# Kernel tuning notes

Measured on AMD Instinct MI355X. Metric: run time of the kernel, lower is better.

Reference implementation:

```python
import jax, jax.numpy as jnp
import numpy as np

B, S, D, H, DK, F, K = 8, 1024, 512, 8, 64, 2048, 31
EPS = 1e-5


def _ln(x, g, b):
    m = jnp.mean(x, -1, keepdims=True)
    v = jnp.mean((x - m) ** 2, -1, keepdims=True)
    return (x - m) * jax.lax.rsqrt(v + EPS) * g + b


def _ff(x, w1, b1, w2, b2):
    return jnp.maximum(x @ w1 + b1, 0.0) @ w2 + b2


def setup_inputs() -> dict:
    key = jax.random.key(0)
    ks = jax.random.split(key, 16)
    w = lambda k, shape: jax.random.normal(k, shape, dtype=jnp.float32) * 0.02
    inp = {"x": jax.random.normal(ks[0], (B, S, D), dtype=jnp.float32)}
    for name in ["norm1", "norm2", "norm3", "norm4", "conv_ln"]:
        inp[name + "_g"] = jnp.ones((D,), jnp.float32)
        inp[name + "_b"] = jnp.zeros((D,), jnp.float32)
    # feed-forward 1 and 2
    inp["ff1_w1"] = w(ks[1], (D, F)); inp["ff1_b1"] = jnp.zeros((F,), jnp.float32)
    inp["ff1_w2"] = w(ks[2], (F, D)); inp["ff1_b2"] = jnp.zeros((D,), jnp.float32)
    inp["ff2_w1"] = w(ks[3], (D, F)); inp["ff2_b1"] = jnp.zeros((F,), jnp.float32)
    inp["ff2_w2"] = w(ks[4], (F, D)); inp["ff2_b2"] = jnp.zeros((D,), jnp.float32)
    # attention projections ([in, out] layout)
    inp["wq"] = w(ks[5], (D, D)); inp["bq"] = jnp.zeros((D,), jnp.float32)
    inp["wk"] = w(ks[6], (D, D)); inp["bk"] = jnp.zeros((D,), jnp.float32)
    inp["wv"] = w(ks[7], (D, D)); inp["bv"] = jnp.zeros((D,), jnp.float32)
    inp["wo"] = w(ks[8], (D, D)); inp["bo"] = jnp.zeros((D,), jnp.float32)
    # convolution module
    inp["pw1_w"] = w(ks[9], (D, 2 * D)); inp["pw1_b"] = jnp.zeros((2 * D,), jnp.float32)
    inp["dw_w"] = w(ks[10], (D, 1, K)); inp["dw_b"] = jnp.zeros((D,), jnp.float32)
    inp["bn_g"] = jnp.ones((D,), jnp.float32); inp["bn_b"] = jnp.zeros((D,), jnp.float32)
    inp["bn_mean"] = jnp.zeros((D,), jnp.float32); inp["bn_var"] = jnp.ones((D,), jnp.float32)
    inp["pw2_w"] = w(ks[11], (D, D)); inp["pw2_b"] = jnp.zeros((D,), jnp.float32)
    return inp


def _forward(x, norm1_g, norm1_b, norm2_g, norm2_b, norm3_g, norm3_b, norm4_g, norm4_b,
             ff1_w1, ff1_b1, ff1_w2, ff1_b2, wq, bq, wk, bk, wv, bv, wo, bo,
             conv_ln_g, conv_ln_b, pw1_w, pw1_b, dw_w, dw_b,
             bn_g, bn_b, bn_mean, bn_var, pw2_w, pw2_b,
             ff2_w1, ff2_b1, ff2_w2, ff2_b2):
    b, s, _ = x.shape
    # half-step FF1
    x = x + 0.5 * _ff(_ln(x, norm1_g, norm1_b), ff1_w1, ff1_b1, ff1_w2, ff1_b2)
    # multi-head self-attention (pre-norm)
    h = _ln(x, norm2_g, norm2_b)
    q = (h @ wq + bq).reshape(b, s, H, DK)
    k = (h @ wk + bk).reshape(b, s, H, DK)
    v = (h @ wv + bv).reshape(b, s, H, DK)
    scores = jnp.einsum("bqhd,bkhd->bhqk", q, k) / jnp.sqrt(jnp.asarray(DK, x.dtype))
    attn = jax.nn.softmax(scores, axis=-1)
    o = jnp.einsum("bhqk,bkhd->bqhd", attn, v).reshape(b, s, D)
    x = x + (o @ wo + bo)
    # convolution module (pre-norm)
    h = _ln(x, norm3_g, norm3_b)
    h = _ln(h, conv_ln_g, conv_ln_b)
    h = h @ pw1_w + pw1_b                                 # [B,S,2D] pointwise conv1
    h = h[..., :D] * jax.nn.sigmoid(h[..., D:])           # GLU over channels
    h = h.transpose(0, 2, 1)                              # [B,D,S]
    h = jax.lax.conv_general_dilated(
        h, dw_w, window_strides=(1,), padding=((K // 2, K // 2),),
        feature_group_count=D, dimension_numbers=("NCH", "OIH", "NCH")) + dw_b[:, None]
    h = (h - bn_mean[:, None]) * jax.lax.rsqrt(bn_var + EPS)[:, None] * bn_g[:, None] + bn_b[:, None]
    h = h * jax.nn.sigmoid(h)                             # SiLU
    h = jnp.einsum("bcl,co->bol", h, pw2_w) + pw2_b[:, None]
    x = x + h.transpose(0, 2, 1)
    # half-step FF2
    x = x + 0.5 * _ff(_ln(x, norm4_g, norm4_b), ff2_w1, ff2_b1, ff2_w2, ff2_b2)
    return x


def reference(x, norm1_g, norm1_b, norm2_g, norm2_b, norm3_g, norm3_b, norm4_g, norm4_b,
              conv_ln_g, conv_ln_b, ff1_w1, ff1_b1, ff1_w2, ff1_b2,
              ff2_w1, ff2_b1, ff2_w2, ff2_b2, wq, bq, wk, bk, wv, bv, wo, bo,
              pw1_w, pw1_b, dw_w, dw_b, bn_g, bn_b, bn_mean, bn_var, pw2_w, pw2_b):
    return _forward(x, norm1_g, norm1_b, norm2_g, norm2_b, norm3_g, norm3_b, norm4_g, norm4_b,
                    ff1_w1, ff1_b1, ff1_w2, ff1_b2, wq, bq, wk, bk, wv, bv, wo, bo,
                    conv_ln_g, conv_ln_b, pw1_w, pw1_b, dw_w, dw_b,
                    bn_g, bn_b, bn_mean, bn_var, pw2_w, pw2_b,
                    ff2_w1, ff2_b1, ff2_w2, ff2_b2)
```

## Files before the change

kernel.cpp:

```cpp
#include <hip/hip_runtime.h>
#include <math.h>

#define TOK    8192
#define DMODEL 512
#define FDIM   2048
#define NH     8
#define DKH    64
#define SEQ    1024
#define BATCH  8
#define KCONV  31
#define LN_EPS 1e-5f

typedef __attribute__((ext_vector_type(8))) short bf16x8;
typedef __attribute__((ext_vector_type(4))) float f32x4;
typedef unsigned short ushort_t;

__device__ __forceinline__ float sigf(float x) { return 1.0f / (1.0f + __expf(-x)); }

__device__ __forceinline__ unsigned short f2bf(float f) {
  unsigned u = __float_as_uint(f);
  u = u + 0x7fffu + ((u >> 16) & 1u);
  return (unsigned short)(u >> 16);
}
__device__ __forceinline__ unsigned pk2(float a, float b) {
  return (unsigned)f2bf(a) | ((unsigned)f2bf(b) << 16);
}
__device__ __forceinline__ float bf2f(ushort_t u) {
  return __uint_as_float((unsigned)u << 16);
}

__device__ __forceinline__ void xcd_swizzle(int gx, int* bx, int* by) {
  const int nwg = gx * (int)gridDim.y;
  const int cpx = nwg >> 3;
  const int bid = (*by) * gx + (*bx);
  const int wg = (bid & 7) * cpx + (bid >> 3);
  *bx = wg % gx;
  *by = wg / gx;
}

struct WJob { const float* src; ushort_t* dst; int K, N, t0; };
struct WJobs { WJob j[10]; };

__global__ __launch_bounds__(256) void wcast_all(WJobs jobs) {
  __shared__ float tile[32][33];
  const int t = blockIdx.x;
  int i = 0;
#pragma unroll
  for (int k = 1; k < 10; ++k) if (t >= jobs.j[k].t0) i = k;
  const WJob jb = jobs.j[i];
  const int local = t - jb.t0;
  const int ntx = jb.N >> 5;
  const int bx = (local % ntx) * 32, by = (local / ntx) * 32;
  const int tx = threadIdx.x, ty = threadIdx.y;
#pragma unroll
  for (int r = 0; r < 32; r += 8)
    tile[ty + r][tx] = jb.src[(size_t)(by + ty + r) * jb.N + bx + tx];
  __syncthreads();
#pragma unroll
  for (int r = 0; r < 32; r += 8)
    jb.dst[(size_t)(bx + ty + r) * jb.K + by + tx] = f2bf(tile[tx][ty + r]);
}

__global__ void misc_prep(const float* __restrict__ w, float* __restrict__ wT,
                          const float* __restrict__ bq, const float* __restrict__ bk,
                          const float* __restrict__ bv, float* __restrict__ bcat) {
  const int idx = blockIdx.x * 256 + threadIdx.x;
  if (idx < DMODEL * KCONV) {
    const int d = idx / KCONV, k = idx % KCONV;
    wT[k * DMODEL + d] = w[idx];
  } else if (idx < DMODEL * KCONV + 3 * DMODEL) {
    const int c = idx - DMODEL * KCONV;
    bcat[c] = (c < DMODEL) ? bq[c] : (c < 2 * DMODEL ? bk[c - DMODEL] : bv[c - 2 * DMODEL]);
  }
}

template <bool OBF>
__global__ __launch_bounds__(256) void ln_kernel(const float* __restrict__ in,
                                                 const float* __restrict__ g,
                                                 const float* __restrict__ b,
                                                 void* __restrict__ outp) {
  const int wave = threadIdx.x >> 6, lane = threadIdx.x & 63;
  const size_t row = (size_t)blockIdx.x * 4 + wave;
  const float* p = in + row * DMODEL + lane * 8;
  const float4 v0 = *(const float4*)p;
  const float4 v1 = *(const float4*)(p + 4);
  float s  = v0.x + v0.y + v0.z + v0.w + v1.x + v1.y + v1.z + v1.w;
  float ss = v0.x*v0.x + v0.y*v0.y + v0.z*v0.z + v0.w*v0.w
           + v1.x*v1.x + v1.y*v1.y + v1.z*v1.z + v1.w*v1.w;
#pragma unroll
  for (int m = 1; m < 64; m <<= 1) { s += __shfl_xor(s, m); ss += __shfl_xor(ss, m); }
  const float mean = s * (1.0f / DMODEL);
  const float var  = ss * (1.0f / DMODEL) - mean * mean;
  const float rstd = rsqrtf(var + LN_EPS);
  const float4 g0 = *(const float4*)(g + lane * 8);
  const float4 g1 = *(const float4*)(g + lane * 8 + 4);
  const float4 bb0 = *(const float4*)(b + lane * 8);
  const float4 bb1 = *(const float4*)(b + lane * 8 + 4);
  float o[8];
  o[0] = (v0.x - mean) * rstd * g0.x + bb0.x;
  o[1] = (v0.y - mean) * rstd * g0.y + bb0.y;
  o[2] = (v0.z - mean) * rstd * g0.z + bb0.z;
  o[3] = (v0.w - mean) * rstd * g0.w + bb0.w;
  o[4] = (v1.x - mean) * rstd * g1.x + bb1.x;
  o[5] = (v1.y - mean) * rstd * g1.y + bb1.y;
  o[6] = (v1.z - mean) * rstd * g1.z + bb1.z;
  o[7] = (v1.w - mean) * rstd * g1.w + bb1.w;
  if (OBF) {
    uint4 pkv;
    pkv.x = pk2(o[0], o[1]); pkv.y = pk2(o[2], o[3]);
    pkv.z = pk2(o[4], o[5]); pkv.w = pk2(o[6], o[7]);
    *(uint4*)((ushort_t*)outp + row * DMODEL + lane * 8) = pkv;
  } else {
    float4 a, c;
    a.x = o[0]; a.y = o[1]; a.z = o[2]; a.w = o[3];
    c.x = o[4]; c.y = o[5]; c.z = o[6]; c.w = o[7];
    float* q = (float*)outp + row * DMODEL + lane * 8;
    *(float4*)q = a;
    *(float4*)(q + 4) = c;
  }
}

__global__ __launch_bounds__(256) void ln2_kernel(const float* __restrict__ in,
                                                  const float* __restrict__ g1,
                                                  const float* __restrict__ b1,
                                                  const float* __restrict__ g2,
                                                  const float* __restrict__ b2,
                                                  ushort_t* __restrict__ outp) {
  const int wave = threadIdx.x >> 6, lane = threadIdx.x & 63;
  const size_t row = (size_t)blockIdx.x * 4 + wave;
  const float* p = in + row * DMODEL + lane * 8;
  float v[8];
  {
    const float4 v0 = *(const float4*)p;
    const float4 v1 = *(const float4*)(p + 4);
    v[0]=v0.x; v[1]=v0.y; v[2]=v0.z; v[3]=v0.w;
    v[4]=v1.x; v[5]=v1.y; v[6]=v1.z; v[7]=v1.w;
  }
  float s = 0.f, ss = 0.f;
#pragma unroll
  for (int e = 0; e < 8; ++e) { s += v[e]; ss += v[e]*v[e]; }
#pragma unroll
  for (int m = 1; m < 64; m <<= 1) { s += __shfl_xor(s, m); ss += __shfl_xor(ss, m); }
  float mean = s * (1.0f / DMODEL);
  float rstd = rsqrtf(ss * (1.0f / DMODEL) - mean * mean + LN_EPS);
  const float4 ga = *(const float4*)(g1 + lane * 8);
  const float4 gb = *(const float4*)(g1 + lane * 8 + 4);
  const float4 ba = *(const float4*)(b1 + lane * 8);
  const float4 bb = *(const float4*)(b1 + lane * 8 + 4);
  const float gg1[8] = {ga.x,ga.y,ga.z,ga.w,gb.x,gb.y,gb.z,gb.w};
  const float bb1[8] = {ba.x,ba.y,ba.z,ba.w,bb.x,bb.y,bb.z,bb.w};
#pragma unroll
  for (int e = 0; e < 8; ++e) v[e] = (v[e] - mean) * rstd * gg1[e] + bb1[e];
  s = 0.f; ss = 0.f;
#pragma unroll
  for (int e = 0; e < 8; ++e) { s += v[e]; ss += v[e]*v[e]; }
#pragma unroll
  for (int m = 1; m < 64; m <<= 1) { s += __shfl_xor(s, m); ss += __shfl_xor(ss, m); }
  mean = s * (1.0f / DMODEL);
  rstd = rsqrtf(ss * (1.0f / DMODEL) - mean * mean + LN_EPS);
  const float4 gc = *(const float4*)(g2 + lane * 8);
  const float4 gd = *(const float4*)(g2 + lane * 8 + 4);
  const float4 bc = *(const float4*)(b2 + lane * 8);
  const float4 bd = *(const float4*)(b2 + lane * 8 + 4);
  const float gg2[8] = {gc.x,gc.y,gc.z,gc.w,gd.x,gd.y,gd.z,gd.w};
  const float bb2[8] = {bc.x,bc.y,bc.z,bc.w,bd.x,bd.y,bd.z,bd.w};
  float o[8];
#pragma unroll
  for (int e = 0; e < 8; ++e) o[e] = (v[e] - mean) * rstd * gg2[e] + bb2[e];
  uint4 pkv;
  pkv.x = pk2(o[0], o[1]); pkv.y = pk2(o[2], o[3]);
  pkv.z = pk2(o[4], o[5]); pkv.w = pk2(o[6], o[7]);
  *(uint4*)(outp + row * DMODEL + lane * 8) = pkv;
}

template <int TN, int ACT, bool RES, bool OBF, bool QSC>
__global__ __launch_bounds__(256) void gemm_bf16(const ushort_t* __restrict__ A,
                                                 const ushort_t* __restrict__ Bt,
                                                 const float* __restrict__ bias,
                                                 const float* __restrict__ Rp,
                                                 float alpha,
                                                 void* __restrict__ Cout,
                                                 int M, int N, int K) {
  constexpr int NF = TN / 32;
  constexpr int NB = TN / 32;
  __shared__ ushort_t Al[128 * 64];
  __shared__ ushort_t Bl[TN * 64];
  const int t = threadIdx.x;
  const int lane = t & 63;
  const int wid = t >> 6;
  const int wr = wid >> 1, wc = wid & 1;
  int bx = blockIdx.x, by = blockIdx.y;
  xcd_swizzle(gridDim.x, &bx, &by);
  const int m0 = by * 128, n0 = bx * TN;

  f32x4 acc[4][NF];
#pragma unroll
  for (int m = 0; m < 4; ++m)
#pragma unroll
    for (int n = 0; n < NF; ++n) acc[m][n] = (f32x4){0.f, 0.f, 0.f, 0.f};

  const int srow = t >> 3;
  const int scol = (t & 7) * 8;
  const ushort_t* Ag = A + (size_t)(m0 + srow) * K + scol;
  const ushort_t* Bg = Bt + (size_t)(n0 + srow) * K + scol;

  for (int k0 = 0; k0 < K; k0 += 64) {
    __syncthreads();
#pragma unroll
    for (int i = 0; i < 4; ++i) {
      __builtin_amdgcn_global_load_lds(
          (const __attribute__((address_space(1))) unsigned*)(Ag + (size_t)i * 32 * K + k0),
          (__attribute__((address_space(3))) unsigned*)(Al + ((size_t)i * 256 + t) * 8),
          16, 0, 0);
    }
#pragma unroll
    for (int i = 0; i < NB; ++i) {
      __builtin_amdgcn_global_load_lds(
          (const __attribute__((address_space(1))) unsigned*)(Bg + (size_t)i * 32 * K + k0),
          (__attribute__((address_space(3))) unsigned*)(Bl + ((size_t)i * 256 + t) * 8),
          16, 0, 0);
    }
    __syncthreads();

#pragma unroll
    for (int ks = 0; ks < 2; ++ks) {
      const int kk = ks * 32 + (lane >> 4) * 8;
      bf16x8 af[4], bfv[NF];
#pragma unroll
      for (int m = 0; m < 4; ++m)
        af[m] = *(const bf16x8*)(Al + (wr * 64 + m * 16 + (lane & 15)) * 64 + kk);
#pragma unroll
      for (int n = 0; n < NF; ++n)
        bfv[n] = *(const bf16x8*)(Bl + (wc * (TN / 2) + n * 16 + (lane & 15)) * 64 + kk);
#pragma unroll
      for (int m = 0; m < 4; ++m)
#pragma unroll
        for (int n = 0; n < NF; ++n)
          acc[m][n] = __builtin_amdgcn_mfma_f32_16x16x32_bf16(af[m], bfv[n], acc[m][n], 0, 0, 0);
    }
  }

#pragma unroll
  for (int m = 0; m < 4; ++m) {
    const int row_b = m0 + wr * 64 + m * 16 + (lane >> 4) * 4;
#pragma unroll
    for (int n = 0; n < NF; ++n) {
      const int col = n0 + wc * (TN / 2) + n * 16 + (lane & 15);
      const float bv = bias[col];
#pragma unroll
      for (int j = 0; j < 4; ++j) {
        float v = acc[m][n][j] + bv;
        if (ACT == 1) v = fmaxf(v, 0.f);
        if (QSC) v *= (col < DMODEL ? 0.125f : 1.0f);
        const size_t idx = (size_t)(row_b + j) * N + col;
        if (RES) v = Rp[idx] + alpha * v;
        if (OBF) ((ushort_t*)Cout)[idx] = f2bf(v);
        else     ((float*)Cout)[idx] = v;
      }
    }
  }
}

__global__ __launch_bounds__(256) void gemm_glu(const ushort_t* __restrict__ A,
                                                const ushort_t* __restrict__ Bt,
                                                const float* __restrict__ bias,
                                                ushort_t* __restrict__ Cout) {
  __shared__ ushort_t Al[128 * 64];
  __shared__ ushort_t Bl[128 * 64];
  const int t = threadIdx.x;
  const int lane = t & 63;
  const int wid = t >> 6;
  const int wr = wid >> 1, wc = wid & 1;
  int bx = blockIdx.x, by = blockIdx.y;
  xcd_swizzle(gridDim.x, &bx, &by);
  const int m0 = by * 128, n0 = bx * 64;
  const int K = DMODEL, N = DMODEL;

  f32x4 aa[4][2], ag[4][2];
#pragma unroll
  for (int m = 0; m < 4; ++m)
#pragma unroll
    for (int n = 0; n < 2; ++n) {
      aa[m][n] = (f32x4){0.f, 0.f, 0.f, 0.f};
      ag[m][n] = (f32x4){0.f, 0.f, 0.f, 0.f};
    }

  const int srow = t >> 3;
  const int scol = (t & 7) * 8;
  const ushort_t* Ag_ = A + (size_t)(m0 + srow) * K + scol;
  const ushort_t* Ba_ = Bt + (size_t)(n0 + srow) * K + scol;
  const ushort_t* Bg_ = Bt + (size_t)(512 + n0 + srow) * K + scol;

  for (int k0 = 0; k0 < K; k0 += 64) {
    __syncthreads();
#pragma unroll
    for (int i = 0; i < 4; ++i) {
      __builtin_amdgcn_global_load_lds(
          (const __attribute__((address_space(1))) unsigned*)(Ag_ + (size_t)i * 32 * K + k0),
          (__attribute__((address_space(3))) unsigned*)(Al + ((size_t)i * 256 + t) * 8),
          16, 0, 0);
    }
#pragma unroll
    for (int i = 0; i < 2; ++i) {
      __builtin_amdgcn_global_load_lds(
          (const __attribute__((address_space(1))) unsigned*)(Ba_ + (size_t)i * 32 * K + k0),
          (__attribute__((address_space(3))) unsigned*)(Bl + ((size_t)i * 256 + t) * 8),
          16, 0, 0);
      __builtin_amdgcn_global_load_lds(
          (const __attribute__((address_space(1))) unsigned*)(Bg_ + (size_t)i * 32 * K + k0),
          (__attribute__((address_space(3))) unsigned*)(Bl + 64 * 64 + ((size_t)i * 256 + t) * 8),
          16, 0, 0);
    }
    __syncthreads();

#pragma unroll
    for (int ks = 0; ks < 2; ++ks) {
      const int kk = ks * 32 + (lane >> 4) * 8;
      bf16x8 af[4], bfa[2], bfg[2];
#pragma unroll
      for (int m = 0; m < 4; ++m)
        af[m] = *(const bf16x8*)(Al + (wr * 64 + m * 16 + (lane & 15)) * 64 + kk);
#pragma unroll
      for (int n = 0; n < 2; ++n) {
        bfa[n] = *(const bf16x8*)(Bl + (wc * 32 + n * 16 + (lane & 15)) * 64 + kk);
        bfg[n] = *(const bf16x8*)(Bl + (64 + wc * 32 + n * 16 + (lane & 15)) * 64 + kk);
      }
#pragma unroll
      for (int m = 0; m < 4; ++m)
#pragma unroll
        for (int n = 0; n < 2; ++n) {
          aa[m][n] = __builtin_amdgcn_mfma_f32_16x16x32_bf16(af[m], bfa[n], aa[m][n], 0, 0, 0);
          ag[m][n] = __builtin_amdgcn_mfma_f32_16x16x32_bf16(af[m], bfg[n], ag[m][n], 0, 0, 0);
        }
    }
  }

#pragma unroll
  for (int m = 0; m < 4; ++m) {
    const int row_b = m0 + wr * 64 + m * 16 + (lane >> 4) * 4;
#pragma unroll
    for (int n = 0; n < 2; ++n) {
      const int col = n0 + wc * 32 + n * 16 + (lane & 15);
      const float ba_v = bias[col];
      const float bg_v = bias[col + DMODEL];
#pragma unroll
      for (int j = 0; j < 4; ++j) {
        const float av = aa[m][n][j] + ba_v;
        const float gv = ag[m][n][j] + bg_v;
        Cout[(size_t)(row_b + j) * N + col] = f2bf(av * sigf(gv));
      }
    }
  }
}

__global__ __launch_bounds__(256) void vtrans(const ushort_t* __restrict__ QKV,
                                              ushort_t* __restrict__ Vt) {
  __shared__ ushort_t tl[64][72];
  const int st = blockIdx.x;
  const int bh = blockIdx.y;
  const int b = bh >> 3, h = bh & 7;
  const int t = threadIdx.x;
#pragma unroll
  for (int i = 0; i < 2; ++i) {
    const int chunk = i * 256 + t;
    const int sr = chunk >> 3, c8 = (chunk & 7) * 8;
    *(uint4*)&tl[sr][c8] =
        *(const uint4*)(QKV + ((size_t)(b * SEQ + st * 64 + sr) * (3 * DMODEL)) + 2 * DMODEL + h * DKH + c8);
  }
  __syncthreads();
#pragma unroll
  for (int i = 0; i < 2; ++i) {
    const int chunk = i * 256 + t;
    const int dr = chunk >> 3, c8 = (chunk & 7) * 8;
    ushort_t tmp[8];
#pragma unroll
    for (int e = 0; e < 8; ++e) tmp[e] = tl[c8 + e][dr];
    *(uint4*)(Vt + ((size_t)(bh * DKH + dr) * SEQ) + st * 64 + c8) = *(uint4*)tmp;
  }
}

__global__ __launch_bounds__(512) void attn_mfma(const ushort_t* __restrict__ QKV,
                                                 const ushort_t* __restrict__ Vt,
                                                 ushort_t* __restrict__ Om) {
  __shared__ ushort_t Ks[128 * 64];
  __shared__ ushort_t Vs[64 * 128];
  __shared__ ushort_t Ps[128 * 128];
  const int t = threadIdx.x;
  const int l = t & 63;
  const int w = t >> 6;
  const int qb = blockIdx.x, h = blockIdx.y, b = blockIdx.z;
  const size_t rowstr = 3 * DMODEL;
  const size_t baseQ = ((size_t)b * SEQ) * rowstr + (size_t)h * DKH;
  const size_t baseK = baseQ + DMODEL;
  const size_t baseV = (size_t)(b * NH + h) * DKH * SEQ;
  const size_t baseO = ((size_t)b * SEQ) * DMODEL + (size_t)h * DKH;

  bf16x8 qf[2];
  {
    const int qrow = qb * 128 + w * 16 + (l & 15);
    const ushort_t* qp = QKV + baseQ + (size_t)qrow * rowstr + ((l >> 4) * 8);
    qf[0] = *(const bf16x8*)(qp);
    qf[1] = *(const bf16x8*)(qp + 32);
  }

  float mrun[4], lrun[4];
  f32x4 o[4];
#pragma unroll
  for (int j = 0; j < 4; ++j) { mrun[j] = -1e30f; lrun[j] = 0.f; }
#pragma unroll
  for (int n = 0; n < 4; ++n) o[n] = (f32x4){0.f, 0.f, 0.f, 0.f};

  for (int kt = 0; kt < SEQ / 128; ++kt) {
    __syncthreads();
#pragma unroll
    for (int i = 0; i < 2; ++i) {
      const int chunk = i * 512 + t;
      {
        const int r = chunk >> 3, c8 = (chunk & 7) * 8;
        const uint4 kv = *(const uint4*)(QKV + baseK + (size_t)(kt * 128 + r) * rowstr + c8);
        *(uint4*)((char*)Ks + r * 128 + ((c8 * 2) ^ ((r & 7) << 4))) = kv;
      }
      {
        const int r = chunk >> 4, c8 = (chunk & 15) * 8;
        const uint4 vv = *(const uint4*)(Vt + baseV + (size_t)r * SEQ + kt * 128 + c8);
        *(uint4*)((char*)Vs + r * 256 + ((c8 * 2) ^ ((r & 15) << 4))) = vv;
      }
    }
    __syncthreads();

    f32x4 s[8];
#pragma unroll
    for (int n = 0; n < 8; ++n) s[n] = (f32x4){0.f, 0.f, 0.f, 0.f};
#pragma unroll
    for (int ks = 0; ks < 2; ++ks) {
      const int kk = ks * 64 + (l >> 4) * 16;
#pragma unroll
      for (int n = 0; n < 8; ++n) {
        const int krow = n * 16 + (l & 15);
        const bf16x8 kf = *(const bf16x8*)((char*)Ks + krow * 128 + (kk ^ ((krow & 7) << 4)));
        s[n] = __builtin_amdgcn_mfma_f32_16x16x32_bf16(qf[ks], kf, s[n], 0, 0, 0);
      }
    }

#pragma unroll
    for (int j = 0; j < 4; ++j) {
      float r0 = s[0][j];
#pragma unroll
      for (int n = 1; n < 8; ++n) r0 = fmaxf(r0, s[n][j]);
      r0 = fmaxf(r0, __shfl_xor(r0, 1));
      r0 = fmaxf(r0, __shfl_xor(r0, 2));
      r0 = fmaxf(r0, __shfl_xor(r0, 4));
      r0 = fmaxf(r0, __shfl_xor(r0, 8));
      const float mn = fmaxf(mrun[j], r0);
      const float cs = __expf(mrun[j] - mn);
      const int prow = w * 16 + (l >> 4) * 4 + j;
      const int pswz = (prow & 15) << 4;
      float psum = 0.f;
#pragma unroll
      for (int n = 0; n < 8; ++n) {
        const float p = __expf(s[n][j] - mn);
        psum += p;
        const int col2 = (n * 16 + (l & 15)) * 2;
        *(ushort_t*)((char*)Ps + prow * 256 + (col2 ^ pswz)) = f2bf(p);
      }
      psum += __shfl_xor(psum, 1);
      psum += __shfl_xor(psum, 2);
      psum += __shfl_xor(psum, 4);
      psum += __shfl_xor(psum, 8);
      lrun[j] = lrun[j] * cs + psum;
      mrun[j] = mn;
      o[0][j] *= cs; o[1][j] *= cs; o[2][j] *= cs; o[3][j] *= cs;
    }

#pragma unroll
    for (int ks = 0; ks < 4; ++ks) {
      const int kk = ks * 64 + (l >> 4) * 16;
      const int arow = w * 16 + (l & 15);
      const bf16x8 pf = *(const bf16x8*)((char*)Ps + arow * 256 + (kk ^ ((arow & 15) << 4)));
#pragma unroll
      for (int n = 0; n < 4; ++n) {
        const int vrow = n * 16 + (l & 15);
        const bf16x8 vf = *(const bf16x8*)((char*)Vs + vrow * 256 + (kk ^ ((vrow & 15) << 4)));
        o[n] = __builtin_amdgcn_mfma_f32_16x16x32_bf16(pf, vf, o[n], 0, 0, 0);
      }
    }
  }

  float inv[4];
#pragma unroll
  for (int j = 0; j < 4; ++j) inv[j] = 1.0f / lrun[j];
#pragma unroll
  for (int j = 0; j < 4; ++j) {
    const int prow = w * 16 + (l >> 4) * 4 + j;
    const int pswz = (prow & 15) << 4;
#pragma unroll
    for (int n = 0; n < 4; ++n) {
      const int col2 = (n * 16 + (l & 15)) * 2;
      *(ushort_t*)((char*)Ps + prow * 256 + (col2 ^ pswz)) = f2bf(o[n][j] * inv[j]);
    }
  }
  __syncthreads();
#pragma unroll
  for (int i = 0; i < 2; ++i) {
    const int chunk = i * 512 + t;
    const int qr = chunk >> 3, c8 = (chunk & 7) * 8;
    const uint4 ov = *(const uint4*)((char*)Ps + qr * 256 + ((c8 * 2) ^ ((qr & 15) << 4)));
    *(uint4*)(Om + baseO + (size_t)(qb * 128 + qr) * DMODEL + c8) = ov;
  }
}

__global__ __launch_bounds__(256) void dwconv_bn_silu(const ushort_t* __restrict__ in,
                                                      const float* __restrict__ wT,
                                                      const float* __restrict__ dwb,
                                                      const float* __restrict__ bng,
                                                      const float* __restrict__ bnb,
                                                      const float* __restrict__ bnm,
                                                      const float* __restrict__ bnv,
                                                      ushort_t* __restrict__ out) {
  const size_t gid = (size_t)blockIdx.x * 256 + threadIdx.x;
  const int dc = (int)(gid & 127) * 4;
  const int s = (int)((gid >> 7) & (SEQ - 1));
  const int b = (int)(gid >> 17);
  const ushort_t* bp = in + (size_t)b * SEQ * DMODEL;
  float ax = 0.f, ay = 0.f, az = 0.f, aw = 0.f;
#pragma unroll
  for (int k = 0; k < KCONV; ++k) {
    const int ssi = s + k - (KCONV / 2);
    if (ssi < 0 || ssi >= SEQ) continue;
    ushort_t xv[4];
    *(uint2*)xv = *(const uint2*)(bp + (size_t)ssi * DMODEL + dc);
    const float4 w = *(const float4*)(wT + k * DMODEL + dc);
    ax = fmaf(bf2f(xv[0]), w.x, ax); ay = fmaf(bf2f(xv[1]), w.y, ay);
    az = fmaf(bf2f(xv[2]), w.z, az); aw = fmaf(bf2f(xv[3]), w.w, aw);
  }
  const float4 bi = *(const float4*)(dwb + dc);
  const float4 mm = *(const float4*)(bnm + dc);
  const float4 vv = *(const float4*)(bnv + dc);
  const float4 gg = *(const float4*)(bng + dc);
  const float4 b2 = *(const float4*)(bnb + dc);
  float v0 = ax + bi.x, v1 = ay + bi.y, v2 = az + bi.z, v3 = aw + bi.w;
  v0 = (v0 - mm.x) * rsqrtf(vv.x + LN_EPS) * gg.x + b2.x;
  v1 = (v1 - mm.y) * rsqrtf(vv.y + LN_EPS) * gg.y + b2.y;
  v2 = (v2 - mm.z) * rsqrtf(vv.z + LN_EPS) * gg.z + b2.z;
  v3 = (v3 - mm.w) * rsqrtf(vv.w + LN_EPS) * gg.w + b2.w;
  v0 = v0 * sigf(v0); v1 = v1 * sigf(v1); v2 = v2 * sigf(v2); v3 = v3 * sigf(v3);
  uint2 o;
  o.x = pk2(v0, v1); o.y = pk2(v2, v3);
  *(uint2*)&out[(((size_t)b * SEQ + s) * DMODEL) + dc] = o;
}

extern "C" void kernel_launch(void* const* d_in, const int* in_sizes, int n_in,
                              void* d_out, int out_size, void* d_ws, size_t ws_size,
                              hipStream_t stream) {
  const float* x    = (const float*)d_in[0];
  const float* n1g  = (const float*)d_in[1];
  const float* n1b  = (const float*)d_in[2];
  const float* n2g  = (const float*)d_in[3];
  const float* n2b  = (const float*)d_in[4];
  const float* n3g  = (const float*)d_in[5];
  const float* n3b  = (const float*)d_in[6];
  const float* n4g  = (const float*)d_in[7];
  const float* n4b  = (const float*)d_in[8];
  const float* clg  = (const float*)d_in[9];
  const float* clb  = (const float*)d_in[10];
  const float* f1w1 = (const float*)d_in[11];
  const float* f1b1 = (const float*)d_in[12];
  const float* f1w2 = (const float*)d_in[13];
  const float* f1b2 = (const float*)d_in[14];
  const float* f2w1 = (const float*)d_in[15];
  const float* f2b1 = (const float*)d_in[16];
  const float* f2w2 = (const float*)d_in[17];
  const float* f2b2 = (const float*)d_in[18];
  const float* wq   = (const float*)d_in[19];
  const float* bq   = (const float*)d_in[20];
  const float* wk   = (const float*)d_in[21];
  const float* bk   = (const float*)d_in[22];
  const float* wv   = (const float*)d_in[23];
  const float* bv   = (const float*)d_in[24];
  const float* wo   = (const float*)d_in[25];
  const float* bo   = (const float*)d_in[26];
  const float* pw1w = (const float*)d_in[27];
  const float* pw1b = (const float*)d_in[28];
  const float* dww  = (const float*)d_in[29];
  const float* dwb  = (const float*)d_in[30];
  const float* bng  = (const float*)d_in[31];
  const float* bnb  = (const float*)d_in[32];
  const float* bnm  = (const float*)d_in[33];
  const float* bnv  = (const float*)d_in[34];
  const float* pw2w = (const float*)d_in[35];
  const float* pw2b = (const float*)d_in[36];

  char* wsb = (char*)d_ws;
  const size_t MB = 1ull << 20;
  ushort_t* Wbf    = (ushort_t*)(wsb + 0);
  ushort_t* f1w1T  = Wbf + 0;
  ushort_t* f1w2T  = Wbf + (1ull << 20);
  ushort_t* f2w1T  = Wbf + (2ull << 20);
  ushort_t* f2w2T  = Wbf + (3ull << 20);
  ushort_t* wqkvT  = Wbf + (4ull << 20);
  ushort_t* wkT    = wqkvT + (256ull << 10);
  ushort_t* wvT    = wqkvT + (512ull << 10);
  ushort_t* woT    = wqkvT + (768ull << 10);
  ushort_t* pw1T   = Wbf + (5ull << 20);
  ushort_t* pw2T   = Wbf + (5ull << 20) + (512ull << 10);
  float*    WTc    = (float*)(wsb + 12 * MB);
  float*    bcat   = (float*)(wsb + 12 * MB + 128 * 1024);
  ushort_t* Lbf    = (ushort_t*)(wsb + 13 * MB);
  ushort_t* Hbf    = (ushort_t*)(wsb + 21 * MB);
  ushort_t* QKVb   = (ushort_t*)(wsb + 53 * MB);
  ushort_t* Vtb    = (ushort_t*)(wsb + 77 * MB);
  ushort_t* Gbf    = (ushort_t*)(wsb + 53 * MB);
  ushort_t* Obf    = (ushort_t*)(wsb + 85 * MB);
  ushort_t* Cbf    = Obf;
  float* out = (float*)d_out;

  const dim3 blk(256);
  const dim3 blk512(512);
  const dim3 blkT(32, 8);
  const dim3 gLN(TOK / 4);
  const dim3 gFFa(FDIM / 128, TOK / 128);
  const dim3 gFFb(DMODEL / 64, TOK / 128);
  const dim3 gQKV(3 * DMODEL / 128, TOK / 128);
  const dim3 gGLU(DMODEL / 64, TOK / 128);
  const dim3 gAttn(SEQ / 128, NH, BATCH);
  const dim3 gVt(SEQ / 64, BATCH * NH);
  const dim3 gElem(TOK * 128 / 256);

  {
    WJobs jobs;
    const float* srcs[10] = {f1w1, f1w2, f2w1, f2w2, wq, wk, wv, wo, pw1w, pw2w};
    ushort_t* dsts[10] = {f1w1T, f1w2T, f2w1T, f2w2T, wqkvT, wkT, wvT, woT, pw1T, pw2T};
    const int Ks[10] = {512, 2048, 512, 2048, 512, 512, 512, 512, 512, 512};
    const int Ns[10] = {2048, 512, 2048, 512, 512, 512, 512, 512, 1024, 512};
    int t0 = 0;
    for (int i = 0; i < 10; ++i) {
      jobs.j[i].src = srcs[i]; jobs.j[i].dst = dsts[i];
      jobs.j[i].K = Ks[i]; jobs.j[i].N = Ns[i]; jobs.j[i].t0 = t0;
      t0 += (Ks[i] / 32) * (Ns[i] / 32);
    }
    wcast_all<<<t0, blkT, 0, stream>>>(jobs);
  }
  misc_prep<<<68, blk, 0, stream>>>(dww, WTc, bq, bk, bv, bcat);

  ln_kernel<true><<<gLN, blk, 0, stream>>>(x, n1g, n1b, Lbf);
  gemm_bf16<128, 1, false, true,  false><<<gFFa, blk, 0, stream>>>(Lbf, f1w1T, f1b1, nullptr, 0.f, Hbf, TOK, FDIM, DMODEL);
  gemm_bf16<64,  0, true,  false, false><<<gFFb, blk, 0, stream>>>(Hbf, f1w2T, f1b2, x, 0.5f, out, TOK, DMODEL, FDIM);

  ln_kernel<true><<<gLN, blk, 0, stream>>>(out, n2g, n2b, Lbf);
  gemm_bf16<128, 0, false, true,  true ><<<gQKV, blk, 0, stream>>>(Lbf, wqkvT, bcat, nullptr, 0.f, QKVb, TOK, 3 * DMODEL, DMODEL);
  vtrans<<<gVt, blk, 0, stream>>>(QKVb, Vtb);
  attn_mfma<<<gAttn, blk512, 0, stream>>>(QKVb, Vtb, Obf);
  gemm_bf16<64,  0, true,  false, false><<<gFFb, blk, 0, stream>>>(Obf, woT, bo, out, 1.0f, out, TOK, DMODEL, DMODEL);

  ln2_kernel<<<gLN, blk, 0, stream>>>(out, n3g, n3b, clg, clb, Lbf);
  gemm_glu<<<gGLU, blk, 0, stream>>>(Lbf, pw1T, pw1b, Gbf);
  dwconv_bn_silu<<<gElem, blk, 0, stream>>>(Gbf, WTc, dwb, bng, bnb, bnm, bnv, Cbf);
  gemm_bf16<64,  0, true,  false, false><<<gFFb, blk, 0, stream>>>(Cbf, pw2T, pw2b, out, 1.0f, out, TOK, DMODEL, DMODEL);

  ln_kernel<true><<<gLN, blk, 0, stream>>>(out, n4g, n4b, Lbf);
  gemm_bf16<128, 1, false, true,  false><<<gFFa, blk, 0, stream>>>(Lbf, f2w1T, f2b1, nullptr, 0.f, Hbf, TOK, FDIM, DMODEL);
  gemm_bf16<64,  0, true,  false, false><<<gFFb, blk, 0, stream>>>(Hbf, f2w2T, f2b2, out, 0.5f, out, TOK, DMODEL, FDIM);
}
```

Before: 352.2 us.

## Prefetch next K/V tile into registers in attention; fold misc prep into weight cast

The attention kernel now loads the next K and V tiles from global memory into registers while the current tile's QK and PV MFMAs run, so global load latency overlaps compute. It also raises wave priority around the MFMA blocks with s_setprio. Separately, the misc_prep kernel (conv weight transpose, QKV bias concat) is merged into the wcast_all launch to save one kernel launch. The cost is extra live registers in attention, which may lower occupancy.

```diff
diff --git a/kernel.cpp b/kernel.cpp
--- a/kernel.cpp
+++ b/kernel.cpp
@@ -39,11 +39,29 @@
 }
 
 struct WJob { const float* src; ushort_t* dst; int K, N, t0; };
-struct WJobs { WJob j[10]; };
+struct WJobs {
+  WJob j[10];
+  int misc_t0;
+  const float* dww; const float* bq; const float* bk; const float* bv;
+  float* wTc; float* bcat;
+};
 
 __global__ __launch_bounds__(256) void wcast_all(WJobs jobs) {
   __shared__ float tile[32][33];
   const int t = blockIdx.x;
+  const int tx = threadIdx.x, ty = threadIdx.y;
+  if (t >= jobs.misc_t0) {
+    const int idx = (t - jobs.misc_t0) * 256 + ty * 32 + tx;
+    if (idx < DMODEL * KCONV) {
+      const int d = idx / KCONV, k = idx % KCONV;
+      jobs.wTc[k * DMODEL + d] = jobs.dww[idx];
+    } else if (idx < DMODEL * KCONV + 3 * DMODEL) {
+      const int c = idx - DMODEL * KCONV;
+      jobs.bcat[c] = (c < DMODEL) ? jobs.bq[c]
+                    : (c < 2 * DMODEL ? jobs.bk[c - DMODEL] : jobs.bv[c - 2 * DMODEL]);
+    }
+    return;
+  }
   int i = 0;
 #pragma unroll
   for (int k = 1; k < 10; ++k) if (t >= jobs.j[k].t0) i = k;
@@ -51,7 +69,6 @@
   const int local = t - jb.t0;
   const int ntx = jb.N >> 5;
   const int bx = (local % ntx) * 32, by = (local / ntx) * 32;
-  const int tx = threadIdx.x, ty = threadIdx.y;
 #pragma unroll
   for (int r = 0; r < 32; r += 8)
     tile[ty + r][tx] = jb.src[(size_t)(by + ty + r) * jb.N + bx + tx];
@@ -59,19 +76,6 @@
 #pragma unroll
   for (int r = 0; r < 32; r += 8)
     jb.dst[(size_t)(bx + ty + r) * jb.K + by + tx] = f2bf(tile[tx][ty + r]);
-}
-
-__global__ void misc_prep(const float* __restrict__ w, float* __restrict__ wT,
-                          const float* __restrict__ bq, const float* __restrict__ bk,
-                          const float* __restrict__ bv, float* __restrict__ bcat) {
-  const int idx = blockIdx.x * 256 + threadIdx.x;
-  if (idx < DMODEL * KCONV) {
-    const int d = idx / KCONV, k = idx % KCONV;
-    wT[k * DMODEL + d] = w[idx];
-  } else if (idx < DMODEL * KCONV + 3 * DMODEL) {
-    const int c = idx - DMODEL * KCONV;
-    bcat[c] = (c < DMODEL) ? bq[c] : (c < 2 * DMODEL ? bk[c - DMODEL] : bv[c - 2 * DMODEL]);
-  }
 }
 
 template <bool OBF>
@@ -403,6 +407,21 @@
     qf[1] = *(const bf16x8*)(qp + 32);
   }
 
+  const int krr = t >> 3, kcc = (t & 7) * 8;
+  const int vrr = t >> 4, vcc = (t & 15) * 8;
+  uint4 kreg[2], vreg[2];
+
+#define LOADREGS(KT)                                                            \
+  {                                                                             \
+    _Pragma("unroll")                                                           \
+    for (int i = 0; i < 2; ++i) {                                               \
+      kreg[i] = *(const uint4*)(QKV + baseK +                                   \
+                 (size_t)((KT) * 128 + i * 64 + krr) * rowstr + kcc);           \
+      vreg[i] = *(const uint4*)(Vt + baseV +                                    \
+                 (size_t)(i * 32 + vrr) * SEQ + (KT) * 128 + vcc);              \
+    }                                                                           \
+  }
+
   float mrun[4], lrun[4];
   f32x4 o[4];
 #pragma unroll
@@ -410,27 +429,24 @@
 #pragma unroll
   for (int n = 0; n < 4; ++n) o[n] = (f32x4){0.f, 0.f, 0.f, 0.f};
 
+  LOADREGS(0);
+
   for (int kt = 0; kt < SEQ / 128; ++kt) {
     __syncthreads();
 #pragma unroll
     for (int i = 0; i < 2; ++i) {
-      const int chunk = i * 512 + t;
-      {
-        const int r = chunk >> 3, c8 = (chunk & 7) * 8;
-        const uint4 kv = *(const uint4*)(QKV + baseK + (size_t)(kt * 128 + r) * rowstr + c8);
-        *(uint4*)((char*)Ks + r * 128 + ((c8 * 2) ^ ((r & 7) << 4))) = kv;
-      }
-      {
-        const int r = chunk >> 4, c8 = (chunk & 15) * 8;
-        const uint4 vv = *(const uint4*)(Vt + baseV + (size_t)r * SEQ + kt * 128 + c8);
-        *(uint4*)((char*)Vs + r * 256 + ((c8 * 2) ^ ((r & 15) << 4))) = vv;
-      }
+      const int r = i * 64 + krr;
+      *(uint4*)((char*)Ks + r * 128 + ((kcc * 2) ^ ((r & 7) << 4))) = kreg[i];
+      const int rv = i * 32 + vrr;
+      *(uint4*)((char*)Vs + rv * 256 + ((vcc * 2) ^ ((rv & 15) << 4))) = vreg[i];
     }
     __syncthreads();
+    if (kt + 1 < SEQ / 128) LOADREGS(kt + 1);
 
     f32x4 s[8];
 #pragma unroll
     for (int n = 0; n < 8; ++n) s[n] = (f32x4){0.f, 0.f, 0.f, 0.f};
+    __builtin_amdgcn_s_setprio(1);
 #pragma unroll
     for (int ks = 0; ks < 2; ++ks) {
       const int kk = ks * 64 + (l >> 4) * 16;
@@ -441,6 +457,7 @@
         s[n] = __builtin_amdgcn_mfma_f32_16x16x32_bf16(qf[ks], kf, s[n], 0, 0, 0);
       }
     }
+    __builtin_amdgcn_s_setprio(0);
 
 #pragma unroll
     for (int j = 0; j < 4; ++j) {
@@ -472,6 +489,7 @@
       o[0][j] *= cs; o[1][j] *= cs; o[2][j] *= cs; o[3][j] *= cs;
     }
 
+    __builtin_amdgcn_s_setprio(1);
 #pragma unroll
     for (int ks = 0; ks < 4; ++ks) {
       const int kk = ks * 64 + (l >> 4) * 16;
@@ -484,7 +502,9 @@
         o[n] = __builtin_amdgcn_mfma_f32_16x16x32_bf16(pf, vf, o[n], 0, 0, 0);
       }
     }
-  }
+    __builtin_amdgcn_s_setprio(0);
+  }
+#undef LOADREGS
 
   float inv[4];
 #pragma unroll
@@ -638,9 +658,12 @@
       jobs.j[i].K = Ks[i]; jobs.j[i].N = Ns[i]; jobs.j[i].t0 = t0;
       t0 += (Ks[i] / 32) * (Ns[i] / 32);
     }
-    wcast_all<<<t0, blkT, 0, stream>>>(jobs);
-  }
-  misc_prep<<<68, blk, 0, stream>>>(dww, WTc, bq, bk, bv, bcat);
+    jobs.misc_t0 = t0;
+    jobs.dww = dww; jobs.bq = bq; jobs.bk = bk; jobs.bv = bv;
+    jobs.wTc = WTc; jobs.bcat = bcat;
+    const int nmisc = (DMODEL * KCONV + 3 * DMODEL + 255) / 256;
+    wcast_all<<<t0 + nmisc, blkT, 0, stream>>>(jobs);
+  }
 
   ln_kernel<true><<<gLN, blk, 0, stream>>>(x, n1g, n1b, Lbf);
   gemm_bf16<128, 1, false, true,  false><<<gFFa, blk, 0, stream>>>(Lbf, f1w1T, f1b1, nullptr, 0.f, Hbf, TOK, FDIM, DMODEL);
```

Result: slower. 375.3 us (+6.6%).
